# Performance work log

Hardware: AMD Instinct MI355X
Metric: run time of the kernel (lower is better)

The kernel has to match this reference:

```python
import jax, jax.numpy as jnp
import numpy as np

jax.config.update("jax_enable_x64", True)


def expand_bits_10(v):
    # v: uint32 with values in [0, 1023]; spread bits 2 apart (30-bit result)
    x = v.astype(jnp.uint32)
    x = (x | (x << 16)) & jnp.uint32(0x030000FF)
    x = (x | (x << 8)) & jnp.uint32(0x0300F00F)
    x = (x | (x << 4)) & jnp.uint32(0x030C30C3)
    x = (x | (x << 2)) & jnp.uint32(0x09249249)
    return x


def encode_morton(x, y, z):
    xc = jnp.clip(x, 0, 1023).astype(jnp.uint32)
    yc = jnp.clip(y, 0, 1023).astype(jnp.uint32)
    zc = jnp.clip(z, 0, 1023).astype(jnp.uint32)
    return (expand_bits_10(xc) << 2) | (expand_bits_10(yc) << 1) | expand_bits_10(zc)


def setup_inputs() -> dict:
    key = jax.random.key(0)
    k1, k2 = jax.random.split(key)
    M = 500_000
    WORLD = 512.0
    centers = jax.random.uniform(k1, (M, 3), jnp.float32, 0.0, WORLD)
    radii = jax.random.uniform(k2, (M, 1), jnp.float32, 0.2, 1.5)
    return {
        "min_corners": centers - radii,
        "max_corners": centers + radii,
        "global_min": jnp.zeros((3,), jnp.float32),
        "voxel_size": jnp.ones((1,), jnp.float32),
        "grid_size": 512,
        "oversized_threshold": 64,
    }


def reference(min_corners, max_corners, global_min, voxel_size, grid_size, oversized_threshold):
    M = min_corners.shape[0]
    T = oversized_threshold  # max voxels per non-oversized sphere (pad width)
    vs = voxel_size.reshape(())

    def gcoord(p):  # world -> clipped grid coordinate, [M,3] int32
        g = jnp.floor((p - global_min[None, :]) / vs).astype(jnp.int32)
        return jnp.clip(g, 0, grid_size - 1)

    g_min = gcoord(min_corners)
    g_max = gcoord(max_corners)
    extent = g_max - g_min + 1  # [M,3]
    num_vox = extent[:, 0] * extent[:, 1] * extent[:, 2]

    # Pass 1: per-sphere voxel counts, oversized flags
    is_oversized = (num_vox > oversized_threshold).astype(jnp.int32)
    counts = jnp.where(is_oversized == 1, 0, num_vox).astype(jnp.int32)
    offsets = jnp.concatenate(
        [jnp.zeros((1,), jnp.int32), jnp.cumsum(counts).astype(jnp.int32)]
    )  # [M+1] CSR offsets
    total_pairs = offsets[-1]

    # Pass 2: enumerate padded sphere-voxel pairs. Linear index k decomposes
    # into (dx, dy, dz) exactly like the kernel's triple loop (z fastest).
    k = jnp.arange(T, dtype=jnp.int32)[None, :]          # [1,T]
    ez = extent[:, 2:3]
    ey = extent[:, 1:2]
    dz = k % ez
    dy = (k // ez) % ey
    dx = k // (ez * ey)
    valid = k < counts[:, None]                            # [M,T]

    gx = g_min[:, 0:1] + dx
    gy = g_min[:, 1:2] + dy
    gz = g_min[:, 2:3] + dz
    morton = encode_morton(gx, gy, gz).astype(jnp.int64)   # [M,T]

    SENTINEL = jnp.int64(1) << 40  # > any 30-bit morton; sorts to the end
    morton = jnp.where(valid, morton, SENTINEL)
    sid = jnp.where(valid, jnp.arange(M, dtype=jnp.int32)[:, None], -1)

    flat_m = morton.reshape(-1)
    flat_s = sid.reshape(-1)
    order = jnp.argsort(flat_m)  # stable; valid pairs form the sorted prefix
    pairs_morton = flat_m[order]
    pairs_sphere_id = flat_s[order]

    return pairs_morton, pairs_sphere_id, offsets, is_oversized, total_pairs
```

## Files before the change

### kernel.cpp

```cpp
#include <hip/hip_runtime.h>
#include <stdint.h>

typedef uint16_t u16;
typedef uint32_t u32;
typedef uint64_t u64;

#define TPB   256
#define TILE  2048
#define RADIX 512
#define RBITS 9
#define STILE 4096
#define WIN   8

#define SCTPB 512
#define NWAVE 8
#define SSLOT 8
#define NXCD  8

__device__ __forceinline__ int clampi(int v, int lo, int hi){ return v < lo ? lo : (v > hi ? hi : v); }

__device__ __forceinline__ u32 expand10(u32 x){
  x &= 1023u;
  x = (x | (x << 16)) & 0x030000FFu;
  x = (x | (x << 8))  & 0x0300F00Fu;
  x = (x | (x << 4))  & 0x030C30C3u;
  x = (x | (x << 2))  & 0x09249249u;
  return x;
}
__device__ __forceinline__ u32 morton3(int gx, int gy, int gz){
  u32 x = (u32)clampi(gx, 0, 1023);
  u32 y = (u32)clampi(gy, 0, 1023);
  u32 z = (u32)clampi(gz, 0, 1023);
  return (expand10(x) << 2) | (expand10(y) << 1) | expand10(z);
}

struct Box { int a0,a1,a2,e0,e1,e2,nv; };
__device__ __forceinline__ Box boxOf(int i, const float* mn, const float* mx,
                                     float g0, float g1, float g2, float vs, int gs){
  Box b;
  int a0 = clampi((int)floorf((mn[3*i+0] - g0) / vs), 0, gs-1);
  int a1 = clampi((int)floorf((mn[3*i+1] - g1) / vs), 0, gs-1);
  int a2 = clampi((int)floorf((mn[3*i+2] - g2) / vs), 0, gs-1);
  int b0 = clampi((int)floorf((mx[3*i+0] - g0) / vs), 0, gs-1);
  int b1 = clampi((int)floorf((mx[3*i+1] - g1) / vs), 0, gs-1);
  int b2 = clampi((int)floorf((mx[3*i+2] - g2) / vs), 0, gs-1);
  b.a0=a0; b.a1=a1; b.a2=a2;
  b.e0=b0-a0+1; b.e1=b1-a1+1; b.e2=b2-a2+1;
  b.nv = b.e0*b.e1*b.e2;
  return b;
}

__global__ void countK(const float* mn, const float* mx, const float* gmin,
                       const float* vs_p, const int* gs_p, const int* T_p,
                       u32* counts, int* out_ovr, int M){
  int i = blockIdx.x * TPB + threadIdx.x;
  if (i >= M) return;
  float vs = vs_p[0]; int gs = gs_p[0]; int T = T_p[0];
  Box b = boxOf(i, mn, mx, gmin[0], gmin[1], gmin[2], vs, gs);
  int ovr = b.nv > T;
  counts[i] = ovr ? 0u : (u32)b.nv;
  out_ovr[i] = ovr;
}

__global__ void scanAK(const u32* counts, int* out_off, u32* blockSums, int M){
  __shared__ u32 s[TPB];
  int b = blockIdx.x, t = threadIdx.x;
  int base = b * TILE + t * 8;
  u32 incl[8]; u32 run = 0;
  #pragma unroll
  for (int j = 0; j < 8; ++j){
    int g = base + j;
    u32 v = (g < M) ? counts[g] : 0u;
    run += v; incl[j] = run;
  }
  s[t] = run;
  __syncthreads();
  for (int o = 1; o < TPB; o <<= 1){
    u32 x = (t >= o) ? s[t-o] : 0u;
    __syncthreads();
    s[t] += x;
    __syncthreads();
  }
  u32 tbase = s[t] - run;
  #pragma unroll
  for (int j = 0; j < 8; ++j){
    int g = base + j;
    if (g < M) out_off[g+1] = (int)(tbase + incl[j]);
  }
  if (t == TPB-1) blockSums[b] = s[TPB-1];
}

__global__ void scanBK(u32* blockSums, int nb){
  __shared__ u32 s[TPB];
  int t = threadIdx.x;
  u32 run = 0;
  int nch = (nb + TPB - 1) / TPB;
  for (int c = 0; c < nch; ++c){
    int i = c * TPB + t;
    u32 v = (i < nb) ? blockSums[i] : 0u;
    s[t] = v;
    __syncthreads();
    for (int o = 1; o < TPB; o <<= 1){
      u32 x = (t >= o) ? s[t-o] : 0u;
      __syncthreads();
      s[t] += x;
      __syncthreads();
    }
    if (i < nb) blockSums[i] = run + s[t] - v;
    u32 tot = s[TPB-1];
    __syncthreads();
    run += tot;
  }
}

__global__ void scanCK(int* out_off, const u32* blockSums, int M, int* out_total){
  int b = blockIdx.x, t = threadIdx.x;
  u32 add = blockSums[b];
  int base = b * TILE + t * 8;
  #pragma unroll
  for (int j = 0; j < 8; ++j){
    int g = base + j;
    if (g < M){
      int v = out_off[g+1] + (int)add;
      out_off[g+1] = v;
      if (g == M-1) out_total[0] = v;
    }
  }
  if (b == 0 && t == 0) out_off[0] = 0;
}

__global__ void genK(const float* mn, const float* mx, const float* gmin,
                     const float* vs_p, const int* gs_p, const int* T_p,
                     const int* out_off, u64* out, u32* hist0,
                     int maxTiles, int M){
  __shared__ u32 winHist[WIN * RADIX];
  __shared__ int stile0;
  int t = threadIdx.x;
  for (int i = t; i < WIN * RADIX; i += TPB) winHist[i] = 0;
  if (t == 0) stile0 = out_off[blockIdx.x * TPB] >> 12;
  __syncthreads();
  int tile0 = stile0;
  int i = blockIdx.x * TPB + t;
  if (i < M){
    float vs = vs_p[0]; int gs = gs_p[0]; int T = T_p[0];
    Box b = boxOf(i, mn, mx, gmin[0], gmin[1], gmin[2], vs, gs);
    if (b.nv <= T){
      int base = out_off[i];
      int k = 0;
      for (int dx = 0; dx < b.e0; ++dx)
        for (int dy = 0; dy < b.e1; ++dy)
          for (int dz = 0; dz < b.e2; ++dz){
            u32 m = morton3(b.a0 + dx, b.a1 + dy, b.a2 + dz);
            int pos = base + k; ++k;
            out[pos] = ((u64)m << 32) | (u32)i;
            u32 d0 = m & (RADIX-1);
            int rel = (pos >> 12) - tile0;
            if (rel >= 0 && rel < WIN) atomicAdd(&winHist[(rel << 9) + d0], 1u);
            else atomicAdd(&hist0[(size_t)d0 * maxTiles + (pos >> 12)], 1u);
          }
    }
  }
  __syncthreads();
  for (int idx = t; idx < WIN * RADIX; idx += TPB){
    u32 c = winHist[idx];
    if (c){
      int wnd = idx >> 9, d = idx & (RADIX-1);
      atomicAdd(&hist0[(size_t)d * maxTiles + (tile0 + wnd)], c);
    }
  }
}

__global__ void histK(const u64* __restrict__ in, u32* hist,
                      const int* total_p, int maxTiles, int shift){
  __shared__ u32 cnt[RADIX];
  int tile = blockIdx.x, t = threadIdx.x;
  int total = *total_p;
  int numTiles = (total + STILE - 1) / STILE;
  if (tile >= numTiles) return;
  cnt[t] = 0; cnt[t + TPB] = 0;
  __syncthreads();
  const u32* hi = (const u32*)in;
  int base = tile * STILE;
  #pragma unroll
  for (int s = 0; s < STILE / TPB; ++s){
    int j = base + s * TPB + t;
    if (j < total) atomicAdd(&cnt[(hi[2*j+1] >> shift) & (RADIX-1)], 1u);
  }
  __syncthreads();
  for (int d = t; d < RADIX; d += TPB)
    hist[(size_t)d * maxTiles + tile] = cnt[d];
}

__global__ void tileScanK(u32* hist, u32* digitTotal, const int* total_p, int maxTiles){
  __shared__ u32 s[TPB];
  int d = blockIdx.x, t = threadIdx.x;
  int total = *total_p;
  int numTiles = (total + STILE - 1) / STILE;
  u32 running = 0;
  int nch = (numTiles + TPB - 1) / TPB;
  for (int c = 0; c < nch; ++c){
    int i = c * TPB + t;
    u32 v = (i < numTiles) ? hist[(size_t)d * maxTiles + i] : 0u;
    s[t] = v;
    __syncthreads();
    for (int o = 1; o < TPB; o <<= 1){
      u32 x = (t >= o) ? s[t-o] : 0u;
      __syncthreads();
      s[t] += x;
      __syncthreads();
    }
    if (i < numTiles) hist[(size_t)d * maxTiles + i] = running + s[t] - v;
    u32 tot = s[TPB-1];
    __syncthreads();
    running += tot;
  }
  if (t == 0) digitTotal[d] = running;
}

__global__ void digitScanK(const u32* digitTotal, u32* digitBase){
  __shared__ u32 s[RADIX];
  int t = threadIdx.x;
  u32 v = digitTotal[t];
  s[t] = v;
  __syncthreads();
  for (int o = 1; o < RADIX; o <<= 1){
    u32 x = (t >= o) ? s[t-o] : 0u;
    __syncthreads();
    s[t] += x;
    __syncthreads();
  }
  digitBase[t] = s[t] - v;
}

__global__ __launch_bounds__(SCTPB, 4)
void scatterK(const u64* __restrict__ in, u64* __restrict__ out,
              const u32* __restrict__ hist, const u32* __restrict__ digitBase,
              const int* total_p, int maxTiles, int shift){
  __shared__ u64 lin[STILE];
  __shared__ u16 wHist[NWAVE * RADIX];
  __shared__ u16 ridx[STILE];
  __shared__ u32 startS[RADIX];
  __shared__ u32 baseS[RADIX];

  int t = threadIdx.x;
  int total = *total_p;
  int numTiles = (total + STILE - 1) / STILE;

  int bid = blockIdx.x;
  int q = numTiles / NXCD, r = numTiles % NXCD;
  int x = bid & (NXCD - 1), pos = bid >> 3;
  int cnt_x = q + (x < r ? 1 : 0);
  if (pos >= cnt_x) return;
  int tile = (x < r ? x * (q + 1) : r * (q + 1) + (x - r) * q) + pos;

  int lane = t & 63, wave = t >> 6;
  u64 lt = (1ull << lane) - 1ull;
  u16* wh = &wHist[wave << 9];

  for (int i = t; i < NWAVE * RADIX; i += SCTPB) wHist[i] = 0;
  __syncthreads();

  int tbase = tile * STILE;
  int cbase = tbase + (wave << 9);
  u32 rrd[SSLOT];

  #pragma unroll
  for (int s = 0; s < SSLOT; ++s){
    int idx = cbase + (s << 6) + lane;
    bool valid = idx < total;
    u64 e = valid ? in[idx] : 0ull;
    lin[idx - tbase] = e;
    int d = (int)(((u32)(e >> 32)) >> shift) & (RADIX - 1);
    u64 mask = __ballot(valid);
    #pragma unroll
    for (int b = 0; b < RBITS; ++b){
      u64 bal = __ballot((d >> b) & 1);
      mask &= ((d >> b) & 1) ? bal : ~bal;
    }
    u32 lr = (u32)__popcll(mask & lt);
    u32 old = valid ? (u32)wh[d] : 0u;
    if (valid && ((mask & lt) == 0ull)) wh[d] = (u16)(old + (u32)__popcll(mask));
    rrd[s] = ((old + lr) << 16) | (u32)d;
  }
  __syncthreads();

  u32 dcnt;
  {
    int d = t & (RADIX - 1);
    u32 c[NWAVE];
    #pragma unroll
    for (int wv = 0; wv < NWAVE; ++wv) c[wv] = wHist[(wv << 9) + d];
    u32 run = 0;
    #pragma unroll
    for (int wv = 0; wv < NWAVE; ++wv){ u32 cc = c[wv]; wHist[(wv << 9) + d] = (u16)run; run += cc; }
    dcnt = run;
    startS[d] = run;
  }
  __syncthreads();

  {
    u32 v = startS[t];
    baseS[t] = v;
    __syncthreads();
    for (int o = 1; o < RADIX; o <<= 1){
      u32 xv = (t >= o) ? baseS[t-o] : 0u;
      __syncthreads();
      baseS[t] += xv;
      __syncthreads();
    }
    u32 excl = baseS[t] - v;
    __syncthreads();
    startS[t] = excl;
    baseS[t] = digitBase[t] + hist[(size_t)t * maxTiles + tile];
  }
  __syncthreads();

  #pragma unroll
  for (int s = 0; s < SSLOT; ++s){
    int idx = cbase + (s << 6) + lane;
    if (idx < total){
      u32 rd = rrd[s];
      u32 d = rd & (RADIX - 1);
      u32 p = startS[d] + (u32)wh[d] + (rd >> 16);
      ridx[p] = (u16)(idx - tbase);
    }
  }
  __syncthreads();

  int tileElems = total - tbase; if (tileElems > STILE) tileElems = STILE;
  for (int j = t; j < tileElems; j += SCTPB){
    u64 e = lin[ridx[j]];
    u32 key = (u32)(e >> 32);
    int d = (int)((key >> shift) & (RADIX - 1));
    int dest = (int)(baseS[d] + (u32)j - startS[d]);
    out[dest] = e;
  }
}

__global__ void unzipTailK(const u64* __restrict__ buf, int* out_m, int* out_s,
                           const int* total_p, int MT){
  int total = *total_p;
  int base = (blockIdx.x * TILE + threadIdx.x) * 2;
  #pragma unroll
  for (int s = 0; s < 8; ++s){
    int j = base + s * TPB * 2;
    if (j + 1 < MT){
      uint2 vm, vs2;
      if (j + 1 < total){
        u64 e0 = buf[j], e1 = buf[j+1];
        vm = make_uint2((u32)(e0 >> 32), (u32)(e1 >> 32));
        vs2 = make_uint2((u32)e0, (u32)e1);
      } else if (j >= total){
        vm = make_uint2(0u, 0u);
        vs2 = make_uint2(0xFFFFFFFFu, 0xFFFFFFFFu);
      } else {
        u64 e0 = buf[j];
        vm = make_uint2((u32)(e0 >> 32), 0u);
        vs2 = make_uint2((u32)e0, 0xFFFFFFFFu);
      }
      *(uint2*)&out_m[j] = vm;
      *(uint2*)&out_s[j] = vs2;
    } else if (j < MT){
      if (j < total){
        u64 e0 = buf[j];
        out_m[j] = (int)(u32)(e0 >> 32);
        out_s[j] = (int)(u32)e0;
      } else {
        out_m[j] = 0;
        out_s[j] = -1;
      }
    }
  }
}

extern "C" void kernel_launch(void* const* d_in, const int* in_sizes, int n_in,
                              void* d_out, int out_size, void* d_ws, size_t ws_size,
                              hipStream_t stream){
  const float* mn   = (const float*)d_in[0];
  const float* mx   = (const float*)d_in[1];
  const float* gmin = (const float*)d_in[2];
  const float* vs   = (const float*)d_in[3];
  const int*   gs   = (const int*)d_in[4];
  const int*   T_p  = (const int*)d_in[5];

  int M = in_sizes[0] / 3;
  long long S = (long long)out_size - 2LL*M - 2LL;
  int T = (int)(S / (2LL*M));
  int MT = (int)((long long)M * T);

  int* out_m     = (int*)d_out;
  int* out_s     = out_m + MT;
  int* out_off   = out_s + MT;
  int* out_ovr   = out_off + (M + 1);
  int* out_total = out_ovr + M;

  uint8_t* w = (uint8_t*)d_ws;
  size_t off = 0;
  auto alloc = [&](size_t bytes) -> void* {
    size_t p = (off + 255) & ~(size_t)255;
    off = p + bytes;
    return (void*)(w + p);
  };
  int nbA = (M + TILE - 1) / TILE;
  u32* counts     = (u32*)alloc((size_t)M * 4);
  u32* blockSums  = (u32*)alloc((size_t)nbA * 4);
  u32* digitTotal = (u32*)alloc(RADIX * 4);
  u32* digitBase  = (u32*)alloc(RADIX * 4);

  size_t fixed = off + 8192;
  size_t avail = ws_size > fixed ? ws_size - fixed : 0;
  long long cap = (long long)(avail / 14) & ~(long long)(STILE - 1);
  if (cap > MT) cap = MT;
  if (cap < STILE) cap = STILE;
  int maxTiles = (int)(cap / STILE);

  size_t histSz = (size_t)RADIX * maxTiles * 4;
  u32* hist0 = (u32*)alloc(histSz);
  u32* hist1 = (u32*)alloc(histSz);
  u32* hist2 = (u32*)alloc(histSz);
  u64* bufA  = (u64*)alloc((size_t)cap * 8);

  u64* bufB = (u64*)d_out;

  int gM = (M + TPB - 1) / TPB;

  hipMemsetAsync(hist0, 0, histSz, stream);
  countK<<<gM, TPB, 0, stream>>>(mn, mx, gmin, vs, gs, T_p, counts, out_ovr, M);
  scanAK<<<nbA, TPB, 0, stream>>>(counts, out_off, blockSums, M);
  scanBK<<<1, TPB, 0, stream>>>(blockSums, nbA);
  scanCK<<<nbA, TPB, 0, stream>>>(out_off, blockSums, M, out_total);
  genK<<<gM, TPB, 0, stream>>>(mn, mx, gmin, vs, gs, T_p, out_off, bufB, hist0, maxTiles, M);

  tileScanK<<<RADIX, TPB, 0, stream>>>(hist0, digitTotal, out_total, maxTiles);
  digitScanK<<<1, RADIX, 0, stream>>>(digitTotal, digitBase);
  scatterK<<<maxTiles, SCTPB, 0, stream>>>(bufB, bufA, hist0, digitBase, out_total, maxTiles, 0);

  histK<<<maxTiles, TPB, 0, stream>>>(bufA, hist1, out_total, maxTiles, RBITS);
  tileScanK<<<RADIX, TPB, 0, stream>>>(hist1, digitTotal, out_total, maxTiles);
  digitScanK<<<1, RADIX, 0, stream>>>(digitTotal, digitBase);
  scatterK<<<maxTiles, SCTPB, 0, stream>>>(bufA, bufB, hist1, digitBase, out_total, maxTiles, RBITS);

  histK<<<maxTiles, TPB, 0, stream>>>(bufB, hist2, out_total, maxTiles, 2*RBITS);
  tileScanK<<<RADIX, TPB, 0, stream>>>(hist2, digitTotal, out_total, maxTiles);
  digitScanK<<<1, RADIX, 0, stream>>>(digitTotal, digitBase);
  scatterK<<<maxTiles, SCTPB, 0, stream>>>(bufB, bufA, hist2, digitBase, out_total, maxTiles, 2*RBITS);

  unzipTailK<<<(MT + 4095) / 4096, TPB, 0, stream>>>(bufA, out_m, out_s, out_total, MT);
}
```

Baseline: 473.2 us.

## Split radix sort payload into separate key and sphere-id arrays, write final pass directly

Switches the radix sort from packed 64-bit key|id records to separate 32-bit key and sphere-id arrays. The histogram passes can then read only keys with vectorized uint4 loads, and the last scatter writes straight into the output arrays. The unzip kernel becomes a small tail-fill kernel that only pads entries beyond the total. Scatter blocks now each process a chain of four tiles, which cuts the grid size. The cost is more workspace (four buffers instead of one plus the output) and two separate scattered writes per element instead of one 8-byte write.

```diff
diff --git a/kernel.cpp b/kernel.cpp
--- a/kernel.cpp
+++ b/kernel.cpp
@@ -5,17 +5,18 @@
 typedef uint32_t u32;
 typedef uint64_t u64;
 
-#define TPB   256
-#define TILE  2048
-#define RADIX 512
-#define RBITS 9
-#define STILE 4096
-#define WIN   8
-
-#define SCTPB 512
-#define NWAVE 8
-#define SSLOT 8
-#define NXCD  8
+#define TPB    256
+#define TILE   2048
+#define RADIX  512
+#define RBITS  9
+#define STILE  4096
+#define WIN    8
+
+#define SCTPB  512
+#define NWAVE  8
+#define SSLOT  8
+#define NXCD   8
+#define GCHAIN 4
 
 __device__ __forceinline__ int clampi(int v, int lo, int hi){ return v < lo ? lo : (v > hi ? hi : v); }
 
@@ -131,7 +132,7 @@
 
 __global__ void genK(const float* mn, const float* mx, const float* gmin,
                      const float* vs_p, const int* gs_p, const int* T_p,
-                     const int* out_off, u64* out, u32* hist0,
+                     const int* out_off, u32* keyOut, u32* sidOut, u32* hist0,
                      int maxTiles, int M){
   __shared__ u32 winHist[WIN * RADIX];
   __shared__ int stile0;
@@ -152,7 +153,8 @@
           for (int dz = 0; dz < b.e2; ++dz){
             u32 m = morton3(b.a0 + dx, b.a1 + dy, b.a2 + dz);
             int pos = base + k; ++k;
-            out[pos] = ((u64)m << 32) | (u32)i;
+            keyOut[pos] = m;
+            sidOut[pos] = (u32)i;
             u32 d0 = m & (RADIX-1);
             int rel = (pos >> 12) - tile0;
             if (rel >= 0 && rel < WIN) atomicAdd(&winHist[(rel << 9) + d0], 1u);
@@ -170,7 +172,7 @@
   }
 }
 
-__global__ void histK(const u64* __restrict__ in, u32* hist,
+__global__ void histK(const u32* __restrict__ keys, u32* hist,
                       const int* total_p, int maxTiles, int shift){
   __shared__ u32 cnt[RADIX];
   int tile = blockIdx.x, t = threadIdx.x;
@@ -179,12 +181,23 @@
   if (tile >= numTiles) return;
   cnt[t] = 0; cnt[t + TPB] = 0;
   __syncthreads();
-  const u32* hi = (const u32*)in;
   int base = tile * STILE;
-  #pragma unroll
-  for (int s = 0; s < STILE / TPB; ++s){
-    int j = base + s * TPB + t;
-    if (j < total) atomicAdd(&cnt[(hi[2*j+1] >> shift) & (RADIX-1)], 1u);
+  if (base + STILE <= total){
+    const uint4* k4 = (const uint4*)(keys + base);
+    #pragma unroll
+    for (int s = 0; s < 4; ++s){
+      uint4 v = k4[s * TPB + t];
+      atomicAdd(&cnt[(v.x >> shift) & (RADIX-1)], 1u);
+      atomicAdd(&cnt[(v.y >> shift) & (RADIX-1)], 1u);
+      atomicAdd(&cnt[(v.z >> shift) & (RADIX-1)], 1u);
+      atomicAdd(&cnt[(v.w >> shift) & (RADIX-1)], 1u);
+    }
+  } else {
+    #pragma unroll
+    for (int s = 0; s < 16; ++s){
+      int j = base + s * TPB + t;
+      if (j < total) atomicAdd(&cnt[(keys[j] >> shift) & (RADIX-1)], 1u);
+    }
   }
   __syncthreads();
   for (int d = t; d < RADIX; d += TPB)
@@ -233,10 +246,12 @@
 }
 
 __global__ __launch_bounds__(SCTPB, 4)
-void scatterK(const u64* __restrict__ in, u64* __restrict__ out,
+void scatterK(const u32* __restrict__ keyIn, const u32* __restrict__ sidIn,
+              u32* __restrict__ keyOut, u32* __restrict__ sidOut,
               const u32* __restrict__ hist, const u32* __restrict__ digitBase,
               const int* total_p, int maxTiles, int shift){
-  __shared__ u64 lin[STILE];
+  __shared__ u32 linK[STILE];
+  __shared__ u32 linS[STILE];
   __shared__ u16 wHist[NWAVE * RADIX];
   __shared__ u16 ridx[STILE];
   __shared__ u32 startS[RADIX];
@@ -245,131 +260,121 @@
   int t = threadIdx.x;
   int total = *total_p;
   int numTiles = (total + STILE - 1) / STILE;
+  int numGroups = (numTiles + GCHAIN - 1) / GCHAIN;
 
   int bid = blockIdx.x;
-  int q = numTiles / NXCD, r = numTiles % NXCD;
+  int q = numGroups >> 3, r = numGroups & (NXCD - 1);
   int x = bid & (NXCD - 1), pos = bid >> 3;
   int cnt_x = q + (x < r ? 1 : 0);
   if (pos >= cnt_x) return;
-  int tile = (x < r ? x * (q + 1) : r * (q + 1) + (x - r) * q) + pos;
+  int group = (x < r ? x * (q + 1) : r * (q + 1) + (x - r) * q) + pos;
 
   int lane = t & 63, wave = t >> 6;
   u64 lt = (1ull << lane) - 1ull;
   u16* wh = &wHist[wave << 9];
 
-  for (int i = t; i < NWAVE * RADIX; i += SCTPB) wHist[i] = 0;
-  __syncthreads();
-
-  int tbase = tile * STILE;
-  int cbase = tbase + (wave << 9);
-  u32 rrd[SSLOT];
-
-  #pragma unroll
-  for (int s = 0; s < SSLOT; ++s){
-    int idx = cbase + (s << 6) + lane;
-    bool valid = idx < total;
-    u64 e = valid ? in[idx] : 0ull;
-    lin[idx - tbase] = e;
-    int d = (int)(((u32)(e >> 32)) >> shift) & (RADIX - 1);
-    u64 mask = __ballot(valid);
+  for (int g = 0; g < GCHAIN; ++g){
+    int tile = group * GCHAIN + g;
+    if (tile >= numTiles) return;
+    __syncthreads();
+    for (int i = t; i < NWAVE * RADIX; i += SCTPB) wHist[i] = 0;
+    __syncthreads();
+
+    int tbase = tile * STILE;
+    int cbase = tbase + (wave << 9);
+    u32 rrd[SSLOT];
+
     #pragma unroll
-    for (int b = 0; b < RBITS; ++b){
-      u64 bal = __ballot((d >> b) & 1);
-      mask &= ((d >> b) & 1) ? bal : ~bal;
-    }
-    u32 lr = (u32)__popcll(mask & lt);
-    u32 old = valid ? (u32)wh[d] : 0u;
-    if (valid && ((mask & lt) == 0ull)) wh[d] = (u16)(old + (u32)__popcll(mask));
-    rrd[s] = ((old + lr) << 16) | (u32)d;
-  }
-  __syncthreads();
-
-  u32 dcnt;
-  {
-    int d = t & (RADIX - 1);
-    u32 c[NWAVE];
+    for (int s = 0; s < SSLOT; ++s){
+      int idx = cbase + (s << 6) + lane;
+      bool valid = idx < total;
+      u32 key = valid ? keyIn[idx] : 0u;
+      u32 sid = valid ? sidIn[idx] : 0u;
+      linK[idx - tbase] = key;
+      linS[idx - tbase] = sid;
+      int d = (int)(key >> shift) & (RADIX - 1);
+      u64 mask = __ballot(valid);
+      #pragma unroll
+      for (int b = 0; b < RBITS; ++b){
+        u64 bal = __ballot((d >> b) & 1);
+        mask &= ((d >> b) & 1) ? bal : ~bal;
+      }
+      u32 lr = (u32)__popcll(mask & lt);
+      u32 old = valid ? (u32)wh[d] : 0u;
+      if (valid && ((mask & lt) == 0ull)) wh[d] = (u16)(old + (u32)__popcll(mask));
+      rrd[s] = ((old + lr) << 16) | (u32)d;
+    }
+    __syncthreads();
+
+    {
+      int d = t;
+      u32 run = 0;
+      #pragma unroll
+      for (int wv = 0; wv < NWAVE; ++wv){
+        u32 cc = wHist[(wv << 9) + d];
+        wHist[(wv << 9) + d] = (u16)run;
+        run += cc;
+      }
+      startS[d] = run;
+    }
+    __syncthreads();
+
+    {
+      u32 v = startS[t];
+      baseS[t] = v;
+      __syncthreads();
+      for (int o = 1; o < RADIX; o <<= 1){
+        u32 xv = (t >= o) ? baseS[t-o] : 0u;
+        __syncthreads();
+        baseS[t] += xv;
+        __syncthreads();
+      }
+      u32 excl = baseS[t] - v;
+      __syncthreads();
+      startS[t] = excl;
+      baseS[t] = digitBase[t] + hist[(size_t)t * maxTiles + tile];
+    }
+    __syncthreads();
+
     #pragma unroll
-    for (int wv = 0; wv < NWAVE; ++wv) c[wv] = wHist[(wv << 9) + d];
-    u32 run = 0;
-    #pragma unroll
-    for (int wv = 0; wv < NWAVE; ++wv){ u32 cc = c[wv]; wHist[(wv << 9) + d] = (u16)run; run += cc; }
-    dcnt = run;
-    startS[d] = run;
-  }
-  __syncthreads();
-
-  {
-    u32 v = startS[t];
-    baseS[t] = v;
-    __syncthreads();
-    for (int o = 1; o < RADIX; o <<= 1){
-      u32 xv = (t >= o) ? baseS[t-o] : 0u;
-      __syncthreads();
-      baseS[t] += xv;
-      __syncthreads();
-    }
-    u32 excl = baseS[t] - v;
-    __syncthreads();
-    startS[t] = excl;
-    baseS[t] = digitBase[t] + hist[(size_t)t * maxTiles + tile];
-  }
-  __syncthreads();
-
-  #pragma unroll
-  for (int s = 0; s < SSLOT; ++s){
-    int idx = cbase + (s << 6) + lane;
-    if (idx < total){
-      u32 rd = rrd[s];
-      u32 d = rd & (RADIX - 1);
-      u32 p = startS[d] + (u32)wh[d] + (rd >> 16);
-      ridx[p] = (u16)(idx - tbase);
-    }
-  }
-  __syncthreads();
-
-  int tileElems = total - tbase; if (tileElems > STILE) tileElems = STILE;
-  for (int j = t; j < tileElems; j += SCTPB){
-    u64 e = lin[ridx[j]];
-    u32 key = (u32)(e >> 32);
-    int d = (int)((key >> shift) & (RADIX - 1));
-    int dest = (int)(baseS[d] + (u32)j - startS[d]);
-    out[dest] = e;
-  }
-}
-
-__global__ void unzipTailK(const u64* __restrict__ buf, int* out_m, int* out_s,
-                           const int* total_p, int MT){
+    for (int s = 0; s < SSLOT; ++s){
+      int idx = cbase + (s << 6) + lane;
+      if (idx < total){
+        u32 rd = rrd[s];
+        u32 d = rd & (RADIX - 1);
+        u32 p = startS[d] + (u32)wh[d] + (rd >> 16);
+        ridx[p] = (u16)(idx - tbase);
+      }
+    }
+    __syncthreads();
+
+    int tileElems = total - tbase; if (tileElems > STILE) tileElems = STILE;
+    for (int j = t; j < tileElems; j += SCTPB){
+      u16 li = ridx[j];
+      u32 key = linK[li];
+      u32 sid = linS[li];
+      int d = (int)(key >> shift) & (RADIX - 1);
+      int dest = (int)(baseS[d] + (u32)j - startS[d]);
+      keyOut[dest] = key;
+      sidOut[dest] = sid;
+    }
+  }
+}
+
+__global__ void tailK(int* out_m, int* out_s, const int* total_p, int MT){
   int total = *total_p;
-  int base = (blockIdx.x * TILE + threadIdx.x) * 2;
-  #pragma unroll
-  for (int s = 0; s < 8; ++s){
-    int j = base + s * TPB * 2;
-    if (j + 1 < MT){
-      uint2 vm, vs2;
-      if (j + 1 < total){
-        u64 e0 = buf[j], e1 = buf[j+1];
-        vm = make_uint2((u32)(e0 >> 32), (u32)(e1 >> 32));
-        vs2 = make_uint2((u32)e0, (u32)e1);
-      } else if (j >= total){
-        vm = make_uint2(0u, 0u);
-        vs2 = make_uint2(0xFFFFFFFFu, 0xFFFFFFFFu);
-      } else {
-        u64 e0 = buf[j];
-        vm = make_uint2((u32)(e0 >> 32), 0u);
-        vs2 = make_uint2((u32)e0, 0xFFFFFFFFu);
-      }
-      *(uint2*)&out_m[j] = vm;
-      *(uint2*)&out_s[j] = vs2;
-    } else if (j < MT){
-      if (j < total){
-        u64 e0 = buf[j];
-        out_m[j] = (int)(u32)(e0 >> 32);
-        out_s[j] = (int)(u32)e0;
-      } else {
-        out_m[j] = 0;
-        out_s[j] = -1;
-      }
-    }
+  int j = (blockIdx.x * TPB + threadIdx.x) * 4;
+  if (j >= MT) return;
+  if (j >= total){
+    if (j + 3 < MT){
+      *(uint4*)&out_m[j] = make_uint4(0u, 0u, 0u, 0u);
+      *(uint4*)&out_s[j] = make_uint4(0xFFFFFFFFu, 0xFFFFFFFFu, 0xFFFFFFFFu, 0xFFFFFFFFu);
+    } else {
+      for (int k = j; k < MT; ++k){ out_m[k] = 0; out_s[k] = -1; }
+    }
+  } else if (j + 4 > total){
+    int end = (j + 4 < MT) ? j + 4 : MT;
+    for (int k = total; k < end; ++k){ out_m[k] = 0; out_s[k] = -1; }
   }
 }
 
@@ -409,7 +414,7 @@
 
   size_t fixed = off + 8192;
   size_t avail = ws_size > fixed ? ws_size - fixed : 0;
-  long long cap = (long long)(avail / 14) & ~(long long)(STILE - 1);
+  long long cap = (long long)(avail / 18) & ~(long long)(STILE - 1);
   if (cap > MT) cap = MT;
   if (cap < STILE) cap = STILE;
   int maxTiles = (int)(cap / STILE);
@@ -418,32 +423,33 @@
   u32* hist0 = (u32*)alloc(histSz);
   u32* hist1 = (u32*)alloc(histSz);
   u32* hist2 = (u32*)alloc(histSz);
-  u64* bufA  = (u64*)alloc((size_t)cap * 8);
-
-  u64* bufB = (u64*)d_out;
+  u32* keyA  = (u32*)alloc((size_t)cap * 4);
+  u32* sidA  = (u32*)alloc((size_t)cap * 4);
+  u32* keyB  = (u32*)alloc((size_t)cap * 4);
+  u32* sidB  = (u32*)alloc((size_t)cap * 4);
 
   int gM = (M + TPB - 1) / TPB;
+  int scGrid = ((maxTiles + GCHAIN - 1) / GCHAIN + NXCD - 1) & ~(NXCD - 1);
 
   hipMemsetAsync(hist0, 0, histSz, stream);
   countK<<<gM, TPB, 0, stream>>>(mn, mx, gmin, vs, gs, T_p, counts, out_ovr, M);
   scanAK<<<nbA, TPB, 0, stream>>>(counts, out_off, blockSums, M);
   scanBK<<<1, TPB, 0, stream>>>(blockSums, nbA);
   scanCK<<<nbA, TPB, 0, stream>>>(out_off, blockSums, M, out_total);
-  genK<<<gM, TPB, 0, stream>>>(mn, mx, gmin, vs, gs, T_p, out_off, bufB, hist0, maxTiles, M);
+  genK<<<gM, TPB, 0, stream>>>(mn, mx, gmin, vs, gs, T_p, out_off, keyA, sidA, hist0, maxTiles, M);
+  tailK<<<(MT/4 + TPB - 1) / TPB, TPB, 0, stream>>>(out_m, out_s, out_total, MT);
 
   tileScanK<<<RADIX, TPB, 0, stream>>>(hist0, digitTotal, out_total, maxTiles);
   digitScanK<<<1, RADIX, 0, stream>>>(digitTotal, digitBase);
-  scatterK<<<maxTiles, SCTPB, 0, stream>>>(bufB, bufA, hist0, digitBase, out_total, maxTiles, 0);
-
-  histK<<<maxTiles, TPB, 0, stream>>>(bufA, hist1, out_total, maxTiles, RBITS);
+  scatterK<<<scGrid, SCTPB, 0, stream>>>(keyA, sidA, keyB, sidB, hist0, digitBase, out_total, maxTiles, 0);
+
+  histK<<<maxTiles, TPB, 0, stream>>>(keyB, hist1, out_total, maxTiles, RBITS);
   tileScanK<<<RADIX, TPB, 0, stream>>>(hist1, digitTotal, out_total, maxTiles);
   digitScanK<<<1, RADIX, 0, stream>>>(digitTotal, digitBase);
-  scatterK<<<maxTiles, SCTPB, 0, stream>>>(bufA, bufB, hist1, digitBase, out_total, maxTiles, RBITS);
-
-  histK<<<maxTiles, TPB, 0, stream>>>(bufB, hist2, out_total, maxTiles, 2*RBITS);
+  scatterK<<<scGrid, SCTPB, 0, stream>>>(keyB, sidB, keyA, sidA, hist1, digitBase, out_total, maxTiles, RBITS);
+
+  histK<<<maxTiles, TPB, 0, stream>>>(keyA, hist2, out_total, maxTiles, 2*RBITS);
   tileScanK<<<RADIX, TPB, 0, stream>>>(hist2, digitTotal, out_total, maxTiles);
   digitScanK<<<1, RADIX, 0, stream>>>(digitTotal, digitBase);
-  scatterK<<<maxTiles, SCTPB, 0, stream>>>(bufB, bufA, hist2, digitBase, out_total, maxTiles, 2*RBITS);
-
-  unzipTailK<<<(MT + 4095) / 4096, TPB, 0, stream>>>(bufA, out_m, out_s, out_total, MT);
-}
+  scatterK<<<scGrid, SCTPB, 0, stream>>>(keyA, sidA, (u32*)out_m, (u32*)out_s, hist2, digitBase, out_total, maxTiles, 2*RBITS);
+}
```

New measurement: 615.5 us. +30.1%, slower.

## Compute all radix digit totals in generation kernel, drop per-pass digit scans

Applied to the files above, without the earlier changes.

The generation kernel now also builds shared-memory histograms of all three 9-bit digits and flushes them to a global array. A single kernel then scans all three, which removes the three per-pass digitScan launches and the digit-total output of tileScan. The histogram kernel also reads keys with 128-bit loads on full tiles, and the unzip kernel writes 4-wide vectors per thread with a larger block span. The trade-off is three extra shared atomics per generated pair in the generation loop.

```diff
diff --git a/kernel.cpp b/kernel.cpp
--- a/kernel.cpp
+++ b/kernel.cpp
@@ -131,12 +131,14 @@
 
 __global__ void genK(const float* mn, const float* mx, const float* gmin,
                      const float* vs_p, const int* gs_p, const int* T_p,
-                     const int* out_off, u64* out, u32* hist0,
+                     const int* out_off, u64* out, u32* hist0, u32* digitTotalAll,
                      int maxTiles, int M){
   __shared__ u32 winHist[WIN * RADIX];
+  __shared__ u32 digTot[3 * RADIX];
   __shared__ int stile0;
   int t = threadIdx.x;
   for (int i = t; i < WIN * RADIX; i += TPB) winHist[i] = 0;
+  for (int i = t; i < 3 * RADIX; i += TPB) digTot[i] = 0;
   if (t == 0) stile0 = out_off[blockIdx.x * TPB] >> 12;
   __syncthreads();
   int tile0 = stile0;
@@ -154,6 +156,9 @@
             int pos = base + k; ++k;
             out[pos] = ((u64)m << 32) | (u32)i;
             u32 d0 = m & (RADIX-1);
+            atomicAdd(&digTot[d0], 1u);
+            atomicAdd(&digTot[RADIX + ((m >> RBITS) & (RADIX-1))], 1u);
+            atomicAdd(&digTot[2*RADIX + (m >> (2*RBITS))], 1u);
             int rel = (pos >> 12) - tile0;
             if (rel >= 0 && rel < WIN) atomicAdd(&winHist[(rel << 9) + d0], 1u);
             else atomicAdd(&hist0[(size_t)d0 * maxTiles + (pos >> 12)], 1u);
@@ -167,6 +172,28 @@
       int wnd = idx >> 9, d = idx & (RADIX-1);
       atomicAdd(&hist0[(size_t)d * maxTiles + (tile0 + wnd)], c);
     }
+  }
+  for (int idx = t; idx < 3 * RADIX; idx += TPB){
+    u32 c = digTot[idx];
+    if (c) atomicAdd(&digitTotalAll[idx], c);
+  }
+}
+
+__global__ void digitScanAllK(const u32* digitTotalAll, u32* digitBaseAll){
+  __shared__ u32 s[RADIX];
+  int t = threadIdx.x;
+  for (int p = 0; p < 3; ++p){
+    u32 v = digitTotalAll[p*RADIX + t];
+    s[t] = v;
+    __syncthreads();
+    for (int o = 1; o < RADIX; o <<= 1){
+      u32 x = (t >= o) ? s[t-o] : 0u;
+      __syncthreads();
+      s[t] += x;
+      __syncthreads();
+    }
+    digitBaseAll[p*RADIX + t] = s[t] - v;
+    __syncthreads();
   }
 }
 
@@ -179,19 +206,29 @@
   if (tile >= numTiles) return;
   cnt[t] = 0; cnt[t + TPB] = 0;
   __syncthreads();
-  const u32* hi = (const u32*)in;
   int base = tile * STILE;
-  #pragma unroll
-  for (int s = 0; s < STILE / TPB; ++s){
-    int j = base + s * TPB + t;
-    if (j < total) atomicAdd(&cnt[(hi[2*j+1] >> shift) & (RADIX-1)], 1u);
+  if (base + STILE <= total){
+    const uint4* k4 = (const uint4*)(in + base);
+    #pragma unroll
+    for (int s = 0; s < 8; ++s){
+      uint4 v = k4[s * TPB + t];
+      atomicAdd(&cnt[(v.y >> shift) & (RADIX-1)], 1u);
+      atomicAdd(&cnt[(v.w >> shift) & (RADIX-1)], 1u);
+    }
+  } else {
+    const u32* hi = (const u32*)in;
+    #pragma unroll
+    for (int s = 0; s < 16; ++s){
+      int j = base + s * TPB + t;
+      if (j < total) atomicAdd(&cnt[(hi[2*j+1] >> shift) & (RADIX-1)], 1u);
+    }
   }
   __syncthreads();
   for (int d = t; d < RADIX; d += TPB)
     hist[(size_t)d * maxTiles + tile] = cnt[d];
 }
 
-__global__ void tileScanK(u32* hist, u32* digitTotal, const int* total_p, int maxTiles){
+__global__ void tileScanK(u32* hist, const int* total_p, int maxTiles){
   __shared__ u32 s[TPB];
   int d = blockIdx.x, t = threadIdx.x;
   int total = *total_p;
@@ -214,22 +251,6 @@
     __syncthreads();
     running += tot;
   }
-  if (t == 0) digitTotal[d] = running;
-}
-
-__global__ void digitScanK(const u32* digitTotal, u32* digitBase){
-  __shared__ u32 s[RADIX];
-  int t = threadIdx.x;
-  u32 v = digitTotal[t];
-  s[t] = v;
-  __syncthreads();
-  for (int o = 1; o < RADIX; o <<= 1){
-    u32 x = (t >= o) ? s[t-o] : 0u;
-    __syncthreads();
-    s[t] += x;
-    __syncthreads();
-  }
-  digitBase[t] = s[t] - v;
 }
 
 __global__ __launch_bounds__(SCTPB, 4)
@@ -284,16 +305,15 @@
   }
   __syncthreads();
 
-  u32 dcnt;
   {
-    int d = t & (RADIX - 1);
-    u32 c[NWAVE];
-    #pragma unroll
-    for (int wv = 0; wv < NWAVE; ++wv) c[wv] = wHist[(wv << 9) + d];
+    int d = t;
     u32 run = 0;
     #pragma unroll
-    for (int wv = 0; wv < NWAVE; ++wv){ u32 cc = c[wv]; wHist[(wv << 9) + d] = (u16)run; run += cc; }
-    dcnt = run;
+    for (int wv = 0; wv < NWAVE; ++wv){
+      u32 cc = wHist[(wv << 9) + d];
+      wHist[(wv << 9) + d] = (u16)run;
+      run += cc;
+    }
     startS[d] = run;
   }
   __syncthreads();
@@ -340,34 +360,33 @@
 __global__ void unzipTailK(const u64* __restrict__ buf, int* out_m, int* out_s,
                            const int* total_p, int MT){
   int total = *total_p;
-  int base = (blockIdx.x * TILE + threadIdx.x) * 2;
+  int base = blockIdx.x * 8192 + threadIdx.x * 4;
   #pragma unroll
   for (int s = 0; s < 8; ++s){
-    int j = base + s * TPB * 2;
-    if (j + 1 < MT){
-      uint2 vm, vs2;
-      if (j + 1 < total){
-        u64 e0 = buf[j], e1 = buf[j+1];
-        vm = make_uint2((u32)(e0 >> 32), (u32)(e1 >> 32));
-        vs2 = make_uint2((u32)e0, (u32)e1);
-      } else if (j >= total){
-        vm = make_uint2(0u, 0u);
-        vs2 = make_uint2(0xFFFFFFFFu, 0xFFFFFFFFu);
+    int j = base + s * 1024;
+    if (j + 3 < MT && (j + 3 < total || j >= total)){
+      uint4 vm, vsid;
+      if (j + 3 < total){
+        u64 e0 = buf[j], e1 = buf[j+1], e2 = buf[j+2], e3 = buf[j+3];
+        vm   = make_uint4((u32)(e0 >> 32), (u32)(e1 >> 32), (u32)(e2 >> 32), (u32)(e3 >> 32));
+        vsid = make_uint4((u32)e0, (u32)e1, (u32)e2, (u32)e3);
       } else {
-        u64 e0 = buf[j];
-        vm = make_uint2((u32)(e0 >> 32), 0u);
-        vs2 = make_uint2((u32)e0, 0xFFFFFFFFu);
+        vm   = make_uint4(0u, 0u, 0u, 0u);
+        vsid = make_uint4(0xFFFFFFFFu, 0xFFFFFFFFu, 0xFFFFFFFFu, 0xFFFFFFFFu);
       }
-      *(uint2*)&out_m[j] = vm;
-      *(uint2*)&out_s[j] = vs2;
+      *(uint4*)&out_m[j] = vm;
+      *(uint4*)&out_s[j] = vsid;
     } else if (j < MT){
-      if (j < total){
-        u64 e0 = buf[j];
-        out_m[j] = (int)(u32)(e0 >> 32);
-        out_s[j] = (int)(u32)e0;
-      } else {
-        out_m[j] = 0;
-        out_s[j] = -1;
+      int end = (j + 4 < MT) ? j + 4 : MT;
+      for (int k = j; k < end; ++k){
+        if (k < total){
+          u64 e = buf[k];
+          out_m[k] = (int)(u32)(e >> 32);
+          out_s[k] = (int)(u32)e;
+        } else {
+          out_m[k] = 0;
+          out_s[k] = -1;
+        }
       }
     }
   }
@@ -402,10 +421,9 @@
     return (void*)(w + p);
   };
   int nbA = (M + TILE - 1) / TILE;
-  u32* counts     = (u32*)alloc((size_t)M * 4);
-  u32* blockSums  = (u32*)alloc((size_t)nbA * 4);
-  u32* digitTotal = (u32*)alloc(RADIX * 4);
-  u32* digitBase  = (u32*)alloc(RADIX * 4);
+  u32* counts       = (u32*)alloc((size_t)M * 4);
+  u32* blockSums    = (u32*)alloc((size_t)nbA * 4);
+  u32* digitBaseAll = (u32*)alloc(3 * RADIX * 4);
 
   size_t fixed = off + 8192;
   size_t avail = ws_size > fixed ? ws_size - fixed : 0;
@@ -415,7 +433,8 @@
   int maxTiles = (int)(cap / STILE);
 
   size_t histSz = (size_t)RADIX * maxTiles * 4;
-  u32* hist0 = (u32*)alloc(histSz);
+  u32* hist0         = (u32*)alloc(histSz + 3 * RADIX * 4);
+  u32* digitTotalAll = (u32*)((uint8_t*)hist0 + histSz);
   u32* hist1 = (u32*)alloc(histSz);
   u32* hist2 = (u32*)alloc(histSz);
   u64* bufA  = (u64*)alloc((size_t)cap * 8);
@@ -424,26 +443,24 @@
 
   int gM = (M + TPB - 1) / TPB;
 
-  hipMemsetAsync(hist0, 0, histSz, stream);
+  hipMemsetAsync(hist0, 0, histSz + 3 * RADIX * 4, stream);
   countK<<<gM, TPB, 0, stream>>>(mn, mx, gmin, vs, gs, T_p, counts, out_ovr, M);
   scanAK<<<nbA, TPB, 0, stream>>>(counts, out_off, blockSums, M);
   scanBK<<<1, TPB, 0, stream>>>(blockSums, nbA);
   scanCK<<<nbA, TPB, 0, stream>>>(out_off, blockSums, M, out_total);
-  genK<<<gM, TPB, 0, stream>>>(mn, mx, gmin, vs, gs, T_p, out_off, bufB, hist0, maxTiles, M);
-
-  tileScanK<<<RADIX, TPB, 0, stream>>>(hist0, digitTotal, out_total, maxTiles);
-  digitScanK<<<1, RADIX, 0, stream>>>(digitTotal, digitBase);
-  scatterK<<<maxTiles, SCTPB, 0, stream>>>(bufB, bufA, hist0, digitBase, out_total, maxTiles, 0);
+  genK<<<gM, TPB, 0, stream>>>(mn, mx, gmin, vs, gs, T_p, out_off, bufB, hist0, digitTotalAll, maxTiles, M);
+  digitScanAllK<<<1, RADIX, 0, stream>>>(digitTotalAll, digitBaseAll);
+
+  tileScanK<<<RADIX, TPB, 0, stream>>>(hist0, out_total, maxTiles);
+  scatterK<<<maxTiles, SCTPB, 0, stream>>>(bufB, bufA, hist0, digitBaseAll + 0*RADIX, out_total, maxTiles, 0);
 
   histK<<<maxTiles, TPB, 0, stream>>>(bufA, hist1, out_total, maxTiles, RBITS);
-  tileScanK<<<RADIX, TPB, 0, stream>>>(hist1, digitTotal, out_total, maxTiles);
-  digitScanK<<<1, RADIX, 0, stream>>>(digitTotal, digitBase);
-  scatterK<<<maxTiles, SCTPB, 0, stream>>>(bufA, bufB, hist1, digitBase, out_total, maxTiles, RBITS);
+  tileScanK<<<RADIX, TPB, 0, stream>>>(hist1, out_total, maxTiles);
+  scatterK<<<maxTiles, SCTPB, 0, stream>>>(bufA, bufB, hist1, digitBaseAll + 1*RADIX, out_total, maxTiles, RBITS);
 
   histK<<<maxTiles, TPB, 0, stream>>>(bufB, hist2, out_total, maxTiles, 2*RBITS);
-  tileScanK<<<RADIX, TPB, 0, stream>>>(hist2, digitTotal, out_total, maxTiles);
-  digitScanK<<<1, RADIX, 0, stream>>>(digitTotal, digitBase);
-  scatterK<<<maxTiles, SCTPB, 0, stream>>>(bufB, bufA, hist2, digitBase, out_total, maxTiles, 2*RBITS);
-
-  unzipTailK<<<(MT + 4095) / 4096, TPB, 0, stream>>>(bufA, out_m, out_s, out_total, MT);
-}
+  tileScanK<<<RADIX, TPB, 0, stream>>>(hist2, out_total, maxTiles);
+  scatterK<<<maxTiles, SCTPB, 0, stream>>>(bufB, bufA, hist2, digitBaseAll + 2*RADIX, out_total, maxTiles, 2*RBITS);
+
+  unzipTailK<<<(MT + 8191) / 8192, TPB, 0, stream>>>(bufA, out_m, out_s, out_total, MT);
+}
```

Result: slower. 501.9 us (+6.1%).
